# Kernel tuning notes

Measured on AMD Instinct MI355X. Metric: run time of the kernel, lower is better.

## Reference

```python
import jax, jax.numpy as jnp
import numpy as np

TOP_K = 8


def setup_inputs() -> dict:
    key = jax.random.key(0)
    k1, k2 = jax.random.split(key)
    B, S, D, E = 4, 4096, 2048, 64
    x = jax.random.normal(k1, (B, S, D), dtype=jnp.float32)
    # nn.Linear(d_model, n_experts): weight [E, D], bias [E]
    W = jax.random.normal(k2, (E, D), dtype=jnp.float32) * (1.0 / np.sqrt(D))
    b = jnp.zeros((E,), dtype=jnp.float32)
    return {"x": x, "W": W, "b": b}


def reference(x, W, b):
    # logits: [B, S, E] = x @ W^T + b
    logits = jnp.einsum("bsd,ed->bse", x, W) + b
    scores = jax.nn.sigmoid(logits)                      # [B, S, E]
    B, S, E = scores.shape
    flat = scores.reshape(B * S, E)                      # tokens x experts
    top_w, top_idx = jax.lax.top_k(flat, TOP_K)          # [B*S, k]
    return top_w.reshape(B, S, TOP_K), top_idx.reshape(B, S, TOP_K)
```

## Files before the change

kernel.cpp:

```cpp
#include <hip/hip_runtime.h>
#include <math.h>

#define TOKENS 16384
#define DMODEL 2048
#define NEXP   64
#define TOPK   8
#define BM     32
#define BK     64
#define NCHUNK (DMODEL / BK)
#define WCHUNKB 24576
#define WSHORTS 12288

typedef unsigned short u16;
typedef float f32x4 __attribute__((ext_vector_type(4)));
typedef short s16x8 __attribute__((ext_vector_type(8)));

__device__ __forceinline__ u16 f2bf(float f, float& back) {
    unsigned u = __float_as_uint(f);
    unsigned r = u + 0x7fffu + ((u >> 16) & 1u);
    back = __uint_as_float(r & 0xffff0000u);
    return (u16)(r >> 16);
}

__global__ __launch_bounds__(256) void wconv(
    const float* __restrict__ W, u16* __restrict__ wimg)
{
    const int id  = blockIdx.x * 256 + threadIdx.x;
    const int e   = id >> 8;
    const int ko8 = id & 255;
    const int k0  = ko8 * 8;
    const int c   = ko8 >> 3;
    const int ks  = (ko8 >> 2) & 1;
    const int hi  = ko8 & 3;
    const int lane = hi * 16 + (e & 15);
    const int eq   = e >> 4;

    const float* src = W + (size_t)e * DMODEL + k0;
    const float4 f0 = *(const float4*)(src);
    const float4 f1 = *(const float4*)(src + 4);
    const float xe[8] = {f0.x, f0.y, f0.z, f0.w, f1.x, f1.y, f1.z, f1.w};
    s16x8 va, vb, vc;
#pragma unroll
    for (int j = 0; j < 8; ++j) {
        float b1, b2, b3;
        const u16 a1 = f2bf(xe[j], b1);
        const float d1 = xe[j] - b1;
        const u16 a2 = f2bf(d1, b2);
        const float d2 = d1 - b2;
        const u16 a3 = f2bf(d2, b3);
        va[j] = (short)a1; vb[j] = (short)a2; vc[j] = (short)a3;
    }
    u16* base = wimg + (size_t)c * WSHORTS + lane * 8;
    *(s16x8*)(base + ((0 * 2 + ks) * 4 + eq) * 512) = va;
    *(s16x8*)(base + ((1 * 2 + ks) * 4 + eq) * 512) = vb;
    *(s16x8*)(base + ((2 * 2 + ks) * 4 + eq) * 512) = vc;
}

__global__ __launch_bounds__(256) void router_fused(
    const float* __restrict__ x, const u16* __restrict__ wimg,
    const float* __restrict__ bias, float* __restrict__ out_w,
    float* __restrict__ out_i)
{
    __shared__ __align__(16) u16 ws[2][WSHORTS];

    const int tid  = threadIdx.x;
    const int lane = tid & 63;
    const int w    = tid >> 6;
    const int wr   = w >> 1;
    const int wc   = w & 1;
    const size_t tokBase = (size_t)blockIdx.x * BM;

    const int arow = wr * 16 + (lane & 15);
    const float* xrow = x + (tokBase + arow) * (size_t)DMODEL + (lane >> 4) * 8;

    const int eq0 = wc * 2;

    f32x4  acc[2][2];
    double accd[2][4];
#pragma unroll
    for (int i = 0; i < 2; ++i)
#pragma unroll
        for (int j = 0; j < 2; ++j) acc[i][j] = (f32x4){0.f, 0.f, 0.f, 0.f};
#pragma unroll
    for (int j = 0; j < 2; ++j)
#pragma unroll
        for (int r = 0; r < 4; ++r) accd[j][r] = 0.0;

    const char* wg = (const char*)wimg + tid * 16;
    float4 wst[6];
#pragma unroll
    for (int r = 0; r < 6; ++r) wst[r] = *(const float4*)(wg + r * 4096);
    float4 xv[4];
#pragma unroll
    for (int ks = 0; ks < 2; ++ks) {
        xv[ks * 2 + 0] = *(const float4*)(xrow + ks * 32);
        xv[ks * 2 + 1] = *(const float4*)(xrow + ks * 32 + 4);
    }
    {
        char* wl = (char*)&ws[0][0] + tid * 16;
#pragma unroll
        for (int r = 0; r < 6; ++r) *(float4*)(wl + r * 4096) = wst[r];
    }
    __syncthreads();

    for (int t = 0; t < NCHUNK; ++t) {
        s16x8 af[3][2];
#pragma unroll
        for (int ks = 0; ks < 2; ++ks) {
            const float xe[8] = {xv[ks * 2].x,     xv[ks * 2].y,
                                 xv[ks * 2].z,     xv[ks * 2].w,
                                 xv[ks * 2 + 1].x, xv[ks * 2 + 1].y,
                                 xv[ks * 2 + 1].z, xv[ks * 2 + 1].w};
#pragma unroll
            for (int j = 0; j < 8; ++j) {
                float b1, b2, b3;
                const u16 a1 = f2bf(xe[j], b1);
                const float d1 = xe[j] - b1;
                const u16 a2 = f2bf(d1, b2);
                const float d2 = d1 - b2;
                const u16 a3 = f2bf(d2, b3);
                af[0][ks][j] = (short)a1;
                af[1][ks][j] = (short)a2;
                af[2][ks][j] = (short)a3;
            }
        }
        if (t + 1 < NCHUNK) {
            const float* xp = xrow + (size_t)(t + 1) * BK;
#pragma unroll
            for (int ks = 0; ks < 2; ++ks) {
                xv[ks * 2 + 0] = *(const float4*)(xp + ks * 32);
                xv[ks * 2 + 1] = *(const float4*)(xp + ks * 32 + 4);
            }
            const char* wgp = wg + (size_t)(t + 1) * WCHUNKB;
#pragma unroll
            for (int r = 0; r < 6; ++r) wst[r] = *(const float4*)(wgp + r * 4096);
        }
        const u16* wb = &ws[t & 1][0];
#pragma unroll
        for (int ks = 0; ks < 2; ++ks) {
#pragma unroll
            for (int nt = 0; nt < 2; ++nt) {
                const u16* bp = wb + (size_t)(eq0 + nt) * 512 + lane * 8;
                const s16x8 b1 = *(const s16x8*)(bp + ((0 * 2 + ks) * 4) * 512);
                const s16x8 b2 = *(const s16x8*)(bp + ((1 * 2 + ks) * 4) * 512);
                const s16x8 b3 = *(const s16x8*)(bp + ((2 * 2 + ks) * 4) * 512);
                f32x4 t0 = acc[ks][nt];
                t0 = __builtin_amdgcn_mfma_f32_16x16x32_bf16(af[0][ks], b1, t0, 0, 0, 0);
                t0 = __builtin_amdgcn_mfma_f32_16x16x32_bf16(af[0][ks], b2, t0, 0, 0, 0);
                t0 = __builtin_amdgcn_mfma_f32_16x16x32_bf16(af[1][ks], b1, t0, 0, 0, 0);
                t0 = __builtin_amdgcn_mfma_f32_16x16x32_bf16(af[0][ks], b3, t0, 0, 0, 0);
                t0 = __builtin_amdgcn_mfma_f32_16x16x32_bf16(af[2][ks], b1, t0, 0, 0, 0);
                t0 = __builtin_amdgcn_mfma_f32_16x16x32_bf16(af[1][ks], b2, t0, 0, 0, 0);
                acc[ks][nt] = t0;
            }
        }
#pragma unroll
        for (int nt = 0; nt < 2; ++nt)
#pragma unroll
            for (int r = 0; r < 4; ++r) {
                accd[nt][r] += (double)acc[0][nt][r] + (double)acc[1][nt][r];
                acc[0][nt][r] = 0.f;
                acc[1][nt][r] = 0.f;
            }
        if (t + 1 < NCHUNK) {
            char* wl = (char*)&ws[(t + 1) & 1][0] + tid * 16;
#pragma unroll
            for (int r = 0; r < 6; ++r) *(float4*)(wl + r * 4096) = wst[r];
        }
        __syncthreads();
    }

    float* lg = (float*)&ws[0][0];
#pragma unroll
    for (int nt = 0; nt < 2; ++nt)
#pragma unroll
        for (int r = 0; r < 4; ++r) {
            const int row = wr * 16 + (lane >> 4) * 4 + r;
            const int col = wc * 32 + nt * 16 + (lane & 15);
            lg[row * 68 + col] = (float)accd[nt][r];
        }
    __syncthreads();

    const float be = bias[lane];
#pragma unroll
    for (int i = 0; i < 8; ++i) {
        const int tl = w * 8 + i;
        float v = lg[tl * 68 + lane] + be;
        const int myi = lane;
        float bv = 0.0f; int bi = 0;
#pragma unroll
        for (int r = 0; r < TOPK; ++r) {
            float mv = v; int mi = myi;
#pragma unroll
            for (int off = 32; off > 0; off >>= 1) {
                const float ov = __shfl_xor(mv, off, 64);
                const int   oi = __shfl_xor(mi, off, 64);
                if (ov > mv || (ov == mv && oi < mi)) { mv = ov; mi = oi; }
            }
            if (lane == r) { bv = mv; bi = mi; }
            if (myi == mi) { v = -INFINITY; }
        }
        if (lane < TOPK) {
            const size_t tok = tokBase + tl;
            out_w[tok * TOPK + lane] = 1.0f / (1.0f + expf(-bv));
            out_i[tok * TOPK + lane] = (float)bi;
        }
    }
}

extern "C" void kernel_launch(void* const* d_in, const int* in_sizes, int n_in,
                              void* d_out, int out_size, void* d_ws, size_t ws_size,
                              hipStream_t stream) {
    const float* x    = (const float*)d_in[0];
    const float* W    = (const float*)d_in[1];
    const float* bias = (const float*)d_in[2];
    float* out_w = (float*)d_out;
    float* out_i = (float*)d_out + (size_t)TOKENS * TOPK;
    u16* wimg = (u16*)d_ws;

    wconv<<<dim3((NEXP * DMODEL / 8) / 256), 256, 0, stream>>>(W, wimg);
    router_fused<<<dim3(TOKENS / BM), 256, 0, stream>>>(x, wimg, bias, out_w, out_i);
}
```

Baseline: 249.6 us.

## Split K across warps, drop LDS weight staging and barriers, halve token tile

Each block now handles 16 tokens, with warp pairs splitting the reduction dimension in half and combining partial double sums through shared memory. Weight fragments are read directly from global/L2 into registers instead of being double-buffered through LDS with per-chunk barriers. The grid doubles and launch bounds request higher occupancy, aiming to hide latency and remove sync stalls. In exchange, L2 traffic for the weight image roughly doubles and weight loads are no longer prefetched.

```diff
diff --git a/kernel.cpp b/kernel.cpp
--- a/kernel.cpp
+++ b/kernel.cpp
@@ -5,10 +5,6 @@
 #define DMODEL 2048
 #define NEXP   64
 #define TOPK   8
-#define BM     32
-#define BK     64
-#define NCHUNK (DMODEL / BK)
-#define WCHUNKB 24576
 #define WSHORTS 12288
 
 typedef unsigned short u16;
@@ -56,24 +52,25 @@
     *(s16x8*)(base + ((2 * 2 + ks) * 4 + eq) * 512) = vc;
 }
 
-__global__ __launch_bounds__(256) void router_fused(
+__global__ __launch_bounds__(256, 4) void router_fused(
     const float* __restrict__ x, const u16* __restrict__ wimg,
     const float* __restrict__ bias, float* __restrict__ out_w,
     float* __restrict__ out_i)
 {
-    __shared__ __align__(16) u16 ws[2][WSHORTS];
+    __shared__ double lg[2][16][NEXP];
 
     const int tid  = threadIdx.x;
     const int lane = tid & 63;
     const int w    = tid >> 6;
-    const int wr   = w >> 1;
-    const int wc   = w & 1;
-    const size_t tokBase = (size_t)blockIdx.x * BM;
-
-    const int arow = wr * 16 + (lane & 15);
-    const float* xrow = x + (tokBase + arow) * (size_t)DMODEL + (lane >> 4) * 8;
-
-    const int eq0 = wc * 2;
+    const int eh   = w & 1;
+    const int kh   = w >> 1;
+    const size_t tokBase = (size_t)blockIdx.x * 16;
+
+    const int arow = lane & 15;
+    const float* xrow = x + (tokBase + arow) * (size_t)DMODEL + kh * 1024 +
+                        (lane >> 4) * 8;
+    const u16* wt0 = wimg + (size_t)kh * 16 * WSHORTS +
+                     (size_t)(eh * 2) * 512 + lane * 8;
 
     f32x4  acc[2][2];
     double accd[2][4];
@@ -86,24 +83,24 @@
 #pragma unroll
         for (int r = 0; r < 4; ++r) accd[j][r] = 0.0;
 
-    const char* wg = (const char*)wimg + tid * 16;
-    float4 wst[6];
-#pragma unroll
-    for (int r = 0; r < 6; ++r) wst[r] = *(const float4*)(wg + r * 4096);
     float4 xv[4];
-#pragma unroll
-    for (int ks = 0; ks < 2; ++ks) {
-        xv[ks * 2 + 0] = *(const float4*)(xrow + ks * 32);
-        xv[ks * 2 + 1] = *(const float4*)(xrow + ks * 32 + 4);
-    }
-    {
-        char* wl = (char*)&ws[0][0] + tid * 16;
-#pragma unroll
-        for (int r = 0; r < 6; ++r) *(float4*)(wl + r * 4096) = wst[r];
-    }
-    __syncthreads();
-
-    for (int t = 0; t < NCHUNK; ++t) {
+    xv[0] = *(const float4*)(xrow);
+    xv[1] = *(const float4*)(xrow + 4);
+    xv[2] = *(const float4*)(xrow + 32);
+    xv[3] = *(const float4*)(xrow + 36);
+
+    for (int t = 0; t < 16; ++t) {
+        const u16* wt = wt0 + (size_t)t * WSHORTS;
+        s16x8 b[3][2][2];
+#pragma unroll
+        for (int tau = 0; tau < 3; ++tau)
+#pragma unroll
+            for (int ks = 0; ks < 2; ++ks)
+#pragma unroll
+                for (int nt = 0; nt < 2; ++nt)
+                    b[tau][ks][nt] = *(const s16x8*)(
+                        wt + ((tau * 2 + ks) * 4 + nt) * 512);
+
         s16x8 af[3][2];
 #pragma unroll
         for (int ks = 0; ks < 2; ++ks) {
@@ -124,36 +121,26 @@
                 af[2][ks][j] = (short)a3;
             }
         }
-        if (t + 1 < NCHUNK) {
-            const float* xp = xrow + (size_t)(t + 1) * BK;
-#pragma unroll
-            for (int ks = 0; ks < 2; ++ks) {
-                xv[ks * 2 + 0] = *(const float4*)(xp + ks * 32);
-                xv[ks * 2 + 1] = *(const float4*)(xp + ks * 32 + 4);
-            }
-            const char* wgp = wg + (size_t)(t + 1) * WCHUNKB;
-#pragma unroll
-            for (int r = 0; r < 6; ++r) wst[r] = *(const float4*)(wgp + r * 4096);
-        }
-        const u16* wb = &ws[t & 1][0];
-#pragma unroll
-        for (int ks = 0; ks < 2; ++ks) {
+        if (t + 1 < 16) {
+            const float* xp = xrow + (size_t)(t + 1) * 64;
+            xv[0] = *(const float4*)(xp);
+            xv[1] = *(const float4*)(xp + 4);
+            xv[2] = *(const float4*)(xp + 32);
+            xv[3] = *(const float4*)(xp + 36);
+        }
+#pragma unroll
+        for (int ks = 0; ks < 2; ++ks)
 #pragma unroll
             for (int nt = 0; nt < 2; ++nt) {
-                const u16* bp = wb + (size_t)(eq0 + nt) * 512 + lane * 8;
-                const s16x8 b1 = *(const s16x8*)(bp + ((0 * 2 + ks) * 4) * 512);
-                const s16x8 b2 = *(const s16x8*)(bp + ((1 * 2 + ks) * 4) * 512);
-                const s16x8 b3 = *(const s16x8*)(bp + ((2 * 2 + ks) * 4) * 512);
                 f32x4 t0 = acc[ks][nt];
-                t0 = __builtin_amdgcn_mfma_f32_16x16x32_bf16(af[0][ks], b1, t0, 0, 0, 0);
-                t0 = __builtin_amdgcn_mfma_f32_16x16x32_bf16(af[0][ks], b2, t0, 0, 0, 0);
-                t0 = __builtin_amdgcn_mfma_f32_16x16x32_bf16(af[1][ks], b1, t0, 0, 0, 0);
-                t0 = __builtin_amdgcn_mfma_f32_16x16x32_bf16(af[0][ks], b3, t0, 0, 0, 0);
-                t0 = __builtin_amdgcn_mfma_f32_16x16x32_bf16(af[2][ks], b1, t0, 0, 0, 0);
-                t0 = __builtin_amdgcn_mfma_f32_16x16x32_bf16(af[1][ks], b2, t0, 0, 0, 0);
+                t0 = __builtin_amdgcn_mfma_f32_16x16x32_bf16(af[0][ks], b[0][ks][nt], t0, 0, 0, 0);
+                t0 = __builtin_amdgcn_mfma_f32_16x16x32_bf16(af[0][ks], b[1][ks][nt], t0, 0, 0, 0);
+                t0 = __builtin_amdgcn_mfma_f32_16x16x32_bf16(af[1][ks], b[0][ks][nt], t0, 0, 0, 0);
+                t0 = __builtin_amdgcn_mfma_f32_16x16x32_bf16(af[0][ks], b[2][ks][nt], t0, 0, 0, 0);
+                t0 = __builtin_amdgcn_mfma_f32_16x16x32_bf16(af[2][ks], b[0][ks][nt], t0, 0, 0, 0);
+                t0 = __builtin_amdgcn_mfma_f32_16x16x32_bf16(af[1][ks], b[1][ks][nt], t0, 0, 0, 0);
                 acc[ks][nt] = t0;
             }
-        }
 #pragma unroll
         for (int nt = 0; nt < 2; ++nt)
 #pragma unroll
@@ -162,30 +149,23 @@
                 acc[0][nt][r] = 0.f;
                 acc[1][nt][r] = 0.f;
             }
-        if (t + 1 < NCHUNK) {
-            char* wl = (char*)&ws[(t + 1) & 1][0] + tid * 16;
-#pragma unroll
-            for (int r = 0; r < 6; ++r) *(float4*)(wl + r * 4096) = wst[r];
-        }
-        __syncthreads();
     }
 
-    float* lg = (float*)&ws[0][0];
 #pragma unroll
     for (int nt = 0; nt < 2; ++nt)
 #pragma unroll
         for (int r = 0; r < 4; ++r) {
-            const int row = wr * 16 + (lane >> 4) * 4 + r;
-            const int col = wc * 32 + nt * 16 + (lane & 15);
-            lg[row * 68 + col] = (float)accd[nt][r];
+            const int row = (lane >> 4) * 4 + r;
+            const int col = eh * 32 + nt * 16 + (lane & 15);
+            lg[kh][row][col] = accd[nt][r];
         }
     __syncthreads();
 
     const float be = bias[lane];
 #pragma unroll
-    for (int i = 0; i < 8; ++i) {
-        const int tl = w * 8 + i;
-        float v = lg[tl * 68 + lane] + be;
+    for (int i = 0; i < 4; ++i) {
+        const int tl = w * 4 + i;
+        float v = (float)(lg[0][tl][lane] + lg[1][tl][lane]) + be;
         const int myi = lane;
         float bv = 0.0f; int bi = 0;
 #pragma unroll
@@ -219,5 +199,5 @@
     u16* wimg = (u16*)d_ws;
 
     wconv<<<dim3((NEXP * DMODEL / 8) / 256), 256, 0, stream>>>(W, wimg);
-    router_fused<<<dim3(TOKENS / BM), 256, 0, stream>>>(x, wimg, bias, out_w, out_i);
-}
+    router_fused<<<dim3(TOKENS / 16), 256, 0, stream>>>(x, wimg, bias, out_w, out_i);
+}
```

Result: no change. 253.6 us (+1.6%).
